# Performance work log

Hardware: AMD Instinct MI355X
Metric: run time of the kernel (lower is better)

Reference implementation:

```python
import jax, jax.numpy as jnp
import numpy as np

B, N, C = 2, 32768, 512
L, H = 64, 8
DH = C // H
NB = N // L
EG_HID = 16


def setup_inputs() -> dict:
    key = jax.random.key(0)
    ks = jax.random.split(key, 12)
    x = jax.random.normal(ks[0], (B, N, C), dtype=jnp.float32)
    attn_mask = jax.random.randint(ks[1], (NB, L, L), 0, 2, dtype=jnp.int32)
    edge_feats = jax.random.normal(ks[2], (NB, L, L, 4), dtype=jnp.float32)
    s = 1.0 / np.sqrt(C)
    w_qkv = jax.random.normal(ks[3], (C, 3 * C), dtype=jnp.float32) * s
    b_qkv = jnp.zeros((3 * C,), dtype=jnp.float32)
    w_proj = jax.random.normal(ks[4], (C, C), dtype=jnp.float32) * s
    b_proj = jnp.zeros((C,), dtype=jnp.float32)
    w_eg1 = jax.random.normal(ks[5], (4, EG_HID), dtype=jnp.float32) * 0.01
    b_eg1 = jnp.zeros((EG_HID,), dtype=jnp.float32)
    w_eg2 = jax.random.normal(ks[6], (EG_HID, H), dtype=jnp.float32) * 0.01
    b_eg2 = jnp.zeros((H,), dtype=jnp.float32)
    w_blk = jax.random.normal(ks[7], (C, H), dtype=jnp.float32) * 0.01
    b_blk = jnp.zeros((H,), dtype=jnp.float32)
    return {"x": x, "attn_mask": attn_mask, "edge_feats": edge_feats,
            "w_qkv": w_qkv, "b_qkv": b_qkv, "w_proj": w_proj, "b_proj": b_proj,
            "w_eg1": w_eg1, "b_eg1": b_eg1, "w_eg2": w_eg2, "b_eg2": b_eg2,
            "w_blk": w_blk, "b_blk": b_blk}


def reference(x, attn_mask, edge_feats, w_qkv, b_qkv, w_proj, b_proj,
              w_eg1, b_eg1, w_eg2, b_eg2, w_blk, b_blk):
    scale = DH ** -0.5
    x_blk = x.reshape(B, NB, L, C)
    # bias_physics: (B, NB, L, L, 4), expanded across batch
    bias = jnp.broadcast_to(edge_feats[None], (B, NB, L, L, 4))
    idx = jnp.arange(L)
    # zero diagonal, set channel 3 of diagonal to 1
    bias = bias.at[:, :, idx, idx, :].set(0.0)
    bias = bias.at[:, :, idx, idx, 3].set(1.0)
    # mask: (B, NB, L, L); ensure each query row attends to at least itself
    mask = jnp.broadcast_to(attn_mask[None], (B, NB, L, L))
    need_diag = (mask.sum(axis=-1) < 1).astype(mask.dtype)  # (B, NB, L)
    diag = mask[:, :, idx, idx]
    mask = mask.at[:, :, idx, idx].set(jnp.maximum(diag, need_diag))
    # qkv
    qkv = x_blk @ w_qkv + b_qkv  # (B, NB, L, 3C)
    q = qkv[..., :C].reshape(B, NB, L, H, DH)
    k = qkv[..., C:2 * C].reshape(B, NB, L, H, DH)
    v = qkv[..., 2 * C:].reshape(B, NB, L, H, DH)
    scores = jnp.einsum('bnqhd,bnkhd->bnqkh', q, k) * scale
    scores = scores + bias[..., 3:4]
    mask_e = (mask[..., None] == 0)  # (B, NB, L, L, 1)
    scores = jnp.where(mask_e, -jnp.inf, scores)
    attn_probs = jax.nn.softmax(scores, axis=3)
    # edge-gate MLP: 4 -> 16 (exact GELU) -> H
    gate = jax.nn.gelu(bias @ w_eg1 + b_eg1, approximate=False) @ w_eg2 + b_eg2
    gate = jnp.where(mask_e, 0.0, gate)
    combined = attn_probs + gate
    x_mid = jnp.einsum('bnqkh,bnkhd->bnqhd', combined, v)  # (B, NB, L, H, DH)
    # block route token
    block_node = x_blk.mean(axis=2, keepdims=True)  # (B, NB, 1, C)
    v_block = (block_node @ w_qkv + b_qkv)[..., 2 * C:].reshape(B, NB, 1, H, DH)
    g_block = jax.nn.sigmoid(x_blk @ w_blk + b_blk)  # (B, NB, L, H)
    x_mid = x_mid + g_block[..., None] * v_block
    out = x_mid.reshape(B, NB, L, C) @ w_proj + b_proj
    return out.reshape(B, N, C)
```

## Files before the change

kernel.cpp:

```cpp
#include <hip/hip_runtime.h>

typedef unsigned short u16;
typedef __attribute__((ext_vector_type(8))) short bf16x8;
typedef __attribute__((ext_vector_type(4))) float f32x4;

#define NTOK 32768
#define CC 512
#define HH 8
#define LL 64
#define NBLK 512
#define MTOK 65536

__device__ __forceinline__ u16 f2bf(float f) {
    unsigned int u = __float_as_uint(f);
    unsigned int r = u + 0x7fffu + ((u >> 16) & 1u);
    return (u16)(r >> 16);
}
__device__ __forceinline__ float bf2f(u16 h) {
    return __uint_as_float(((unsigned int)h) << 16);
}
__device__ __forceinline__ bf16x8 bc8(uint4 v) {
    return __builtin_bit_cast(bf16x8, v);
}
__device__ __forceinline__ void dma16(const u16* g, u16* l) {
    __builtin_amdgcn_global_load_lds((const __attribute__((address_space(1))) void*)g,
                                     (__attribute__((address_space(3))) void*)l, 16, 0, 0);
}

__global__ __launch_bounds__(256) void convert_gblock_kernel(const float* __restrict__ x,
                                                             u16* __restrict__ xbf,
                                                             const float* __restrict__ w_blk,
                                                             const float* __restrict__ b_blk,
                                                             float* __restrict__ gbl) {
    __shared__ float wbs[4608];
    int tid = threadIdx.x;
    for (int i = tid; i < 4096; i += 256) wbs[i + (i >> 6)] = w_blk[i];
    size_t tok = (size_t)blockIdx.x * 4 + (tid >> 6);
    int lane = tid & 63;
    int c0 = lane * 8;
    const float4* p = (const float4*)(x + tok * CC + c0);
    float4 a = p[0], b = p[1];
    uint4 o;
    o.x = (unsigned)f2bf(a.x) | ((unsigned)f2bf(a.y) << 16);
    o.y = (unsigned)f2bf(a.z) | ((unsigned)f2bf(a.w) << 16);
    o.z = (unsigned)f2bf(b.x) | ((unsigned)f2bf(b.y) << 16);
    o.w = (unsigned)f2bf(b.z) | ((unsigned)f2bf(b.w) << 16);
    *(uint4*)(xbf + tok * CC + c0) = o;
    float xv[8] = {a.x, a.y, a.z, a.w, b.x, b.y, b.z, b.w};
    __syncthreads();
    float acc[8];
#pragma unroll
    for (int h = 0; h < 8; ++h) acc[h] = 0.f;
#pragma unroll
    for (int j = 0; j < 8; ++j) {
        const float* wr = &wbs[(c0 + j) * 8 + lane];
#pragma unroll
        for (int h = 0; h < 8; ++h) acc[h] += xv[j] * wr[h];
    }
#pragma unroll
    for (int h = 0; h < 8; ++h) {
#pragma unroll
        for (int off = 1; off < 64; off <<= 1) acc[h] += __shfl_xor(acc[h], off);
    }
    float v = acc[0];
#pragma unroll
    for (int h = 1; h < 8; ++h) v = (lane == h) ? acc[h] : v;
    if (lane < 8) gbl[tok * 8 + lane] = 1.f / (1.f + __expf(-(v + b_blk[lane])));
}

__global__ __launch_bounds__(256) void transpose_bf16_kernel(const float* __restrict__ in,
                                                             u16* __restrict__ out,
                                                             int K, int Nn) {
    __shared__ float tile[32][33];
    int n0 = blockIdx.x * 32, k0 = blockIdx.y * 32;
    int tx = threadIdx.x & 31, ty = threadIdx.x >> 5;
#pragma unroll
    for (int i = 0; i < 4; ++i)
        tile[ty + i * 8][tx] = in[(size_t)(k0 + ty + i * 8) * Nn + n0 + tx];
    __syncthreads();
#pragma unroll
    for (int i = 0; i < 4; ++i)
        out[(size_t)(n0 + ty + i * 8) * K + k0 + tx] = f2bf(tile[tx][ty + i * 8]);
}

__global__ __launch_bounds__(256) void gate_sbias_kernel(const int* __restrict__ mask,
                                                         const float* __restrict__ edge,
                                                         const float* __restrict__ w1,
                                                         const float* __restrict__ b1,
                                                         const float* __restrict__ w2,
                                                         const float* __restrict__ b2,
                                                         u16* __restrict__ gate2,
                                                         u16* __restrict__ sbias2) {
    __shared__ float w1s[64], b1s[16], w2s[128], b2s[8];
    __shared__ int nds[16];
    int t = threadIdx.x;
    int nb = blockIdx.x >> 2;
    int qt = blockIdx.x & 3;
    if (t < 64) w1s[t] = w1[t];
    if (t < 16) b1s[t] = b1[t];
    if (t < 128) w2s[t] = w2[t];
    if (t < 8) b2s[t] = b2[t];
    if (t >= 128 && t < 144) {
        int q = qt * 16 + (t - 128);
        int s = 0;
        const int* mr = mask + (size_t)(nb * 64 + q) * 64;
#pragma unroll 8
        for (int k = 0; k < 64; ++k) s += mr[k];
        nds[t - 128] = (s < 1) ? 1 : 0;
    }
    __syncthreads();
#pragma unroll 1
    for (int it = 0; it < 4; ++it) {
        int p = it * 256 + t;
        int ql = p >> 6, k = p & 63;
        int q = qt * 16 + ql;
        int pk = (k & 15) * 4 + (k >> 4);
        int mv = mask[(size_t)(nb * 64 + q) * 64 + k];
        float e0, e1, e2, e3;
        if (q == k) {
            mv = max(mv, nds[ql]);
            e0 = e1 = e2 = 0.f;
            e3 = 1.f;
        } else {
            const float* ep = edge + ((size_t)(nb * 64 + q) * 64 + k) * 4;
            e0 = ep[0]; e1 = ep[1]; e2 = ep[2]; e3 = ep[3];
        }
        sbias2[(size_t)(nb * 64 + q) * 64 + pk] = f2bf(mv ? e3 : -1e30f);
        float g[8];
#pragma unroll
        for (int hh = 0; hh < 8; ++hh) g[hh] = b2s[hh];
#pragma unroll
        for (int j = 0; j < 16; ++j) {
            float hpre = e0 * w1s[j] + e1 * w1s[16 + j] + e2 * w1s[32 + j] + e3 * w1s[48 + j] + b1s[j];
            float hg = 0.5f * hpre * (1.f + erff(hpre * 0.70710678f));
#pragma unroll
            for (int hh = 0; hh < 8; ++hh) g[hh] += hg * w2s[j * 8 + hh];
        }
#pragma unroll
        for (int hh = 0; hh < 8; ++hh)
            gate2[(((size_t)nb * 8 + hh) * 64 + q) * 64 + pk] = f2bf(mv ? g[hh] : 0.f);
    }
}

__global__ __launch_bounds__(512, 4) void fused_qkv_attn_kernel(const u16* __restrict__ xbf,
                                                                const u16* __restrict__ wqkvT,
                                                                const float* __restrict__ b_qkv,
                                                                const u16* __restrict__ sbias2,
                                                                const u16* __restrict__ gate2,
                                                                const float* __restrict__ gbl,
                                                                u16* __restrict__ xmid) {
    __shared__ __align__(16) u16 Xs[2][64 * 64];
    __shared__ __align__(16) u16 QPs[2][64 * 72];
    __shared__ __align__(16) u16 Ks[2][64 * 72];
    __shared__ __align__(16) u16 VTs[2][64 * 72];
    __shared__ float gl[2][64], vbl[2][64];

    int tid = threadIdx.x;
    int bidf = blockIdx.x;
    int logical = (bidf & 7) * 512 + (bidf >> 3);
    int hp = logical & 3, nb = (logical >> 2) & 511, b = logical >> 11;
    int wave = tid >> 6, lane = tid & 63, l15 = lane & 15, quad = lane >> 4;
    int hloc = wave >> 2;
    int h = hp * 2 + hloc;
    int nt = wave & 3;
    int m0 = nt * 16;
    size_t blockrow = (size_t)(b * NTOK + nb * 64);

    int srow = tid >> 3;
    int jch = tid & 7;
    int js = jch ^ (srow & 7);
    const u16* gA = xbf + (blockrow + srow) * CC + js * 8;
    int sw = l15 & 7;

    const u16* gB0 = wqkvT + (size_t)(0 * 512 + h * 64 + nt * 16 + l15) * CC;
    const u16* gB1 = wqkvT + (size_t)(1 * 512 + h * 64 + nt * 16 + l15) * CC;
    const u16* gB2 = wqkvT + (size_t)(2 * 512 + h * 64 + nt * 16 + l15) * CC;
    float bq0 = b_qkv[0 * 512 + h * 64 + nt * 16 + l15];
    float bq1 = b_qkv[1 * 512 + h * 64 + nt * 16 + l15];
    float bq2 = b_qkv[2 * 512 + h * 64 + nt * 16 + l15];

    f32x4 accQ[4], accK[4], accV[4];
#pragma unroll
    for (int i = 0; i < 4; ++i) {
        accQ[i] = (f32x4){0.f, 0.f, 0.f, 0.f};
        accK[i] = (f32x4){0.f, 0.f, 0.f, 0.f};
        accV[i] = (f32x4){0.f, 0.f, 0.f, 0.f};
    }

    dma16(gA, &Xs[0][wave * 512]);
    __syncthreads();
    for (int kt = 0; kt < 8; ++kt) {
        int buf = kt & 1;
        if (kt < 7) dma16(gA + (kt + 1) * 64, &Xs[buf ^ 1][wave * 512]);
#pragma unroll
        for (int kk = 0; kk < 2; ++kk) {
            int ch = ((kk * 4 + quad) ^ sw) * 8;
            bf16x8 a[4];
#pragma unroll
            for (int i = 0; i < 4; ++i) a[i] = *(const bf16x8*)&Xs[buf][(i * 16 + l15) * 64 + ch];
            int ko = kt * 64 + kk * 32 + quad * 8;
            bf16x8 b0 = bc8(*(const uint4*)(gB0 + ko));
            bf16x8 b1 = bc8(*(const uint4*)(gB1 + ko));
            bf16x8 b2 = bc8(*(const uint4*)(gB2 + ko));
#pragma unroll
            for (int i = 0; i < 4; ++i) {
                accQ[i] = __builtin_amdgcn_mfma_f32_16x16x32_bf16(a[i], b0, accQ[i], 0, 0, 0);
                accK[i] = __builtin_amdgcn_mfma_f32_16x16x32_bf16(a[i], b1, accK[i], 0, 0, 0);
                accV[i] = __builtin_amdgcn_mfma_f32_16x16x32_bf16(a[i], b2, accV[i], 0, 0, 0);
            }
        }
        __syncthreads();
    }

    {
        int dloc = nt * 16 + l15;
#pragma unroll
        for (int i = 0; i < 4; ++i) {
#pragma unroll
            for (int r = 0; r < 4; ++r) {
                int tok = i * 16 + quad * 4 + r;
                QPs[hloc][tok * 72 + dloc] = f2bf(accQ[i][r] + bq0);
                Ks[hloc][tok * 72 + dloc] = f2bf(accK[i][r] + bq1);
                VTs[hloc][dloc * 72 + tok] = f2bf(accV[i][r] + bq2);
            }
        }
    }
    if (tid < 128) {
        int hl = tid >> 6, tok = tid & 63;
        gl[hl][tok] = gbl[(blockrow + tok) * 8 + hp * 2 + hl];
    }
    __syncthreads();

    if (tid < 128) {
        int hl = tid >> 6, d = tid & 63;
        float s = 0.f;
#pragma unroll 8
        for (int k = 0; k < 64; ++k) s += bf2f(VTs[hl][d * 72 + k]);
        vbl[hl][d] = s * 0.015625f;
    }

    f32x4 sc[4];
#pragma unroll
    for (int t = 0; t < 4; ++t) sc[t] = (f32x4){0.f, 0.f, 0.f, 0.f};
#pragma unroll
    for (int kk = 0; kk < 2; ++kk) {
        bf16x8 a = *(const bf16x8*)&QPs[hloc][(m0 + l15) * 72 + kk * 32 + quad * 8];
#pragma unroll
        for (int t = 0; t < 4; ++t) {
            bf16x8 bb = *(const bf16x8*)&Ks[hloc][(t * 16 + l15) * 72 + kk * 32 + quad * 8];
            sc[t] = __builtin_amdgcn_mfma_f32_16x16x32_bf16(a, bb, sc[t], 0, 0, 0);
        }
    }
    {
        const u16* sb2 = sbias2 + (size_t)nb * 4096;
        const u16* gp2 = gate2 + ((size_t)nb * 8 + h) * 4096;
#pragma unroll
        for (int r = 0; r < 4; ++r) {
            int q = m0 + quad * 4 + r;
            ushort4 sv = *(const ushort4*)(sb2 + (q * 16 + l15) * 4);
            float bias_t[4] = {bf2f(sv.x), bf2f(sv.y), bf2f(sv.z), bf2f(sv.w)};
            float mx = -3e38f;
#pragma unroll
            for (int t = 0; t < 4; ++t) {
                float v = sc[t][r] * 0.125f + bias_t[t];
                sc[t][r] = v;
                mx = fmaxf(mx, v);
            }
            mx = fmaxf(mx, __shfl_xor(mx, 1));
            mx = fmaxf(mx, __shfl_xor(mx, 2));
            mx = fmaxf(mx, __shfl_xor(mx, 4));
            mx = fmaxf(mx, __shfl_xor(mx, 8));
            float sum = 0.f;
#pragma unroll
            for (int t = 0; t < 4; ++t) {
                float p = __expf(sc[t][r] - mx);
                sc[t][r] = p;
                sum += p;
            }
            sum += __shfl_xor(sum, 1);
            sum += __shfl_xor(sum, 2);
            sum += __shfl_xor(sum, 4);
            sum += __shfl_xor(sum, 8);
            float inv = 1.f / sum;
            ushort4 gv = *(const ushort4*)(gp2 + (q * 16 + l15) * 4);
            float gate_t[4] = {bf2f(gv.x), bf2f(gv.y), bf2f(gv.z), bf2f(gv.w)};
#pragma unroll
            for (int t = 0; t < 4; ++t) {
                float comb = sc[t][r] * inv + gate_t[t];
                QPs[hloc][q * 72 + t * 16 + l15] = f2bf(comb);
            }
        }
    }
    __syncthreads();

    f32x4 o[4];
#pragma unroll
    for (int t = 0; t < 4; ++t) o[t] = (f32x4){0.f, 0.f, 0.f, 0.f};
#pragma unroll
    for (int kk = 0; kk < 2; ++kk) {
        bf16x8 a = *(const bf16x8*)&QPs[hloc][(m0 + l15) * 72 + kk * 32 + quad * 8];
#pragma unroll
        for (int t = 0; t < 4; ++t) {
            bf16x8 bb = *(const bf16x8*)&VTs[hloc][(t * 16 + l15) * 72 + kk * 32 + quad * 8];
            o[t] = __builtin_amdgcn_mfma_f32_16x16x32_bf16(a, bb, o[t], 0, 0, 0);
        }
    }
#pragma unroll
    for (int t = 0; t < 4; ++t) {
#pragma unroll
        for (int r = 0; r < 4; ++r) {
            int q = m0 + quad * 4 + r, d = t * 16 + l15;
            float v = o[t][r] + gl[hloc][q] * vbl[hloc][d];
            xmid[(blockrow + q) * CC + h * 64 + d] = f2bf(v);
        }
    }
}

__global__ __launch_bounds__(256) void outproj_kernel(const u16* __restrict__ xmid,
                                                      const u16* __restrict__ wprojT,
                                                      const float* __restrict__ b_proj,
                                                      float* __restrict__ out) {
    __shared__ __align__(16) u16 As[128 * 64], Bs[128 * 64];
    int tid = threadIdx.x;
    int flat = blockIdx.x;
    int logical = (flat & 7) * 256 + (flat >> 3);
    int n0 = (logical & 3) * 128;
    int m0 = (logical >> 2) * 128;
    int lane = tid & 63, l15 = lane & 15, quad = lane >> 4, wave = tid >> 6;
    int r8 = lane >> 3, jch = lane & 7;
    int js = jch ^ r8;
    int mwl = (wave >> 1) * 64, nwl = (wave & 1) * 64;
    int sw = l15 & 7;

    f32x4 acc[4][4];
#pragma unroll
    for (int i = 0; i < 4; ++i)
#pragma unroll
        for (int j = 0; j < 4; ++j) acc[i][j] = (f32x4){0.f, 0.f, 0.f, 0.f};

    int arow[4], brow[4];
#pragma unroll
    for (int i = 0; i < 4; ++i) arow[i] = (mwl + i * 16 + l15) * 64;
#pragma unroll
    for (int j = 0; j < 4; ++j) brow[j] = (nwl + j * 16 + l15) * 64;

    const u16* gA = xmid + (size_t)(m0 + wave * 32 + r8) * CC + js * 8;
    const u16* gB = wprojT + (size_t)(n0 + wave * 32 + r8) * CC + js * 8;
    u16* lA = As + wave * 32 * 64;
    u16* lB = Bs + wave * 32 * 64;

    for (int kt = 0; kt < 8; ++kt) {
        int k0 = kt * 64;
#pragma unroll
        for (int t = 0; t < 4; ++t) {
            dma16(gA + (size_t)t * 8 * CC + k0, lA + t * 8 * 64);
            dma16(gB + (size_t)t * 8 * CC + k0, lB + t * 8 * 64);
        }
        __syncthreads();
#pragma unroll
        for (int kk = 0; kk < 2; ++kk) {
            int ch = ((kk * 4 + quad) ^ sw) * 8;
            bf16x8 a[4], bb[4];
#pragma unroll
            for (int i = 0; i < 4; ++i) a[i] = *(const bf16x8*)&As[arow[i] + ch];
#pragma unroll
            for (int j = 0; j < 4; ++j) bb[j] = *(const bf16x8*)&Bs[brow[j] + ch];
#pragma unroll
            for (int i = 0; i < 4; ++i)
#pragma unroll
                for (int j = 0; j < 4; ++j)
                    acc[i][j] = __builtin_amdgcn_mfma_f32_16x16x32_bf16(a[i], bb[j], acc[i][j], 0, 0, 0);
        }
        __syncthreads();
    }
#pragma unroll
    for (int i = 0; i < 4; ++i)
#pragma unroll
        for (int j = 0; j < 4; ++j) {
            int col = n0 + nwl + j * 16 + l15;
            float bp = b_proj[col];
#pragma unroll
            for (int r = 0; r < 4; ++r) {
                int row = m0 + mwl + i * 16 + quad * 4 + r;
                out[(size_t)row * CC + col] = acc[i][j][r] + bp;
            }
        }
}

extern "C" void kernel_launch(void* const* d_in, const int* in_sizes, int n_in,
                              void* d_out, int out_size, void* d_ws, size_t ws_size,
                              hipStream_t stream) {
    const float* x = (const float*)d_in[0];
    const int* attn_mask = (const int*)d_in[1];
    const float* edge = (const float*)d_in[2];
    const float* w_qkv = (const float*)d_in[3];
    const float* b_qkv = (const float*)d_in[4];
    const float* w_proj = (const float*)d_in[5];
    const float* b_proj = (const float*)d_in[6];
    const float* w_eg1 = (const float*)d_in[7];
    const float* b_eg1 = (const float*)d_in[8];
    const float* w_eg2 = (const float*)d_in[9];
    const float* b_eg2 = (const float*)d_in[10];
    const float* w_blk = (const float*)d_in[11];
    const float* b_blk = (const float*)d_in[12];
    float* out = (float*)d_out;

    char* ws = (char*)d_ws;
    u16* xbf = (u16*)ws;
    u16* xmid = (u16*)(ws + 67108864);
    u16* gate2 = (u16*)(ws + 268435456);
    u16* sbias2 = (u16*)(ws + 301989888);
    u16* wqkvT = (u16*)(ws + 306184192);
    u16* wprojT = (u16*)(ws + 307757056);
    float* gbl = (float*)(ws + 308281344);

    convert_gblock_kernel<<<16384, 256, 0, stream>>>(x, xbf, w_blk, b_blk, gbl);
    transpose_bf16_kernel<<<dim3(48, 16), 256, 0, stream>>>(w_qkv, wqkvT, 512, 1536);
    transpose_bf16_kernel<<<dim3(16, 16), 256, 0, stream>>>(w_proj, wprojT, 512, 512);
    gate_sbias_kernel<<<2048, 256, 0, stream>>>(attn_mask, edge, w_eg1, b_eg1, w_eg2, b_eg2,
                                                gate2, sbias2);
    fused_qkv_attn_kernel<<<4096, 512, 0, stream>>>(xbf, wqkvT, b_qkv, sbias2, gate2, gbl, xmid);
    outproj_kernel<<<2048, 256, 0, stream>>>(xmid, wprojT, b_proj, out);
}
```

Measured before the change: 628.7 us.

## Software-pipeline QKV GEMM weight loads and prefetch bias/gate before softmax

Restructures the fused QKV projection main loop so the global weight fragments for the next k-step are loaded one step ahead into registers. The loop is fully unrolled and __syncthreads is replaced with explicit s_waitcnt vmcnt(3) plus s_barrier, so outstanding weight loads need not drain before the LDS double-buffer barrier. The score-bias and gate loads are also hoisted ahead of the score computation to hide their latency. The cost is higher register pressure, and correctness depends on the hand-counted vmcnt matching the number of in-flight loads.

New measurement: 642.2 us. 1.02x slower.

```diff
diff --git a/kernel.cpp b/kernel.cpp
--- a/kernel.cpp
+++ b/kernel.cpp
@@ -187,29 +187,106 @@
         accV[i] = (f32x4){0.f, 0.f, 0.f, 0.f};
     }
 
+    int koq = quad * 8;
     dma16(gA, &Xs[0][wave * 512]);
-    __syncthreads();
+    asm volatile("" ::: "memory");
+    bf16x8 c0 = bc8(*(const uint4*)(gB0 + koq));
+    bf16x8 c1 = bc8(*(const uint4*)(gB1 + koq));
+    bf16x8 c2 = bc8(*(const uint4*)(gB2 + koq));
+    asm volatile("s_waitcnt vmcnt(3)" ::: "memory");
+    __builtin_amdgcn_s_barrier();
+
+#pragma unroll
     for (int kt = 0; kt < 8; ++kt) {
         int buf = kt & 1;
-        if (kt < 7) dma16(gA + (kt + 1) * 64, &Xs[buf ^ 1][wave * 512]);
-#pragma unroll
-        for (int kk = 0; kk < 2; ++kk) {
-            int ch = ((kk * 4 + quad) ^ sw) * 8;
-            bf16x8 a[4];
-#pragma unroll
-            for (int i = 0; i < 4; ++i) a[i] = *(const bf16x8*)&Xs[buf][(i * 16 + l15) * 64 + ch];
-            int ko = kt * 64 + kk * 32 + quad * 8;
-            bf16x8 b0 = bc8(*(const uint4*)(gB0 + ko));
-            bf16x8 b1 = bc8(*(const uint4*)(gB1 + ko));
-            bf16x8 b2 = bc8(*(const uint4*)(gB2 + ko));
-#pragma unroll
-            for (int i = 0; i < 4; ++i) {
-                accQ[i] = __builtin_amdgcn_mfma_f32_16x16x32_bf16(a[i], b0, accQ[i], 0, 0, 0);
-                accK[i] = __builtin_amdgcn_mfma_f32_16x16x32_bf16(a[i], b1, accK[i], 0, 0, 0);
-                accV[i] = __builtin_amdgcn_mfma_f32_16x16x32_bf16(a[i], b2, accV[i], 0, 0, 0);
-            }
-        }
-        __syncthreads();
+        if (kt < 7) {
+            dma16(gA + (kt + 1) * 64, &Xs[buf ^ 1][wave * 512]);
+            asm volatile("" ::: "memory");
+        }
+        {
+            int ko1 = kt * 64 + 32 + koq;
+            bf16x8 n0 = bc8(*(const uint4*)(gB0 + ko1));
+            bf16x8 n1 = bc8(*(const uint4*)(gB1 + ko1));
+            bf16x8 n2 = bc8(*(const uint4*)(gB2 + ko1));
+            {
+                int ch = (quad ^ sw) * 8;
+                bf16x8 a0 = *(const bf16x8*)&Xs[buf][(0 * 16 + l15) * 64 + ch];
+                bf16x8 a1 = *(const bf16x8*)&Xs[buf][(1 * 16 + l15) * 64 + ch];
+                bf16x8 a2 = *(const bf16x8*)&Xs[buf][(2 * 16 + l15) * 64 + ch];
+                bf16x8 a3 = *(const bf16x8*)&Xs[buf][(3 * 16 + l15) * 64 + ch];
+                accQ[0] = __builtin_amdgcn_mfma_f32_16x16x32_bf16(a0, c0, accQ[0], 0, 0, 0);
+                accK[0] = __builtin_amdgcn_mfma_f32_16x16x32_bf16(a0, c1, accK[0], 0, 0, 0);
+                accV[0] = __builtin_amdgcn_mfma_f32_16x16x32_bf16(a0, c2, accV[0], 0, 0, 0);
+                accQ[1] = __builtin_amdgcn_mfma_f32_16x16x32_bf16(a1, c0, accQ[1], 0, 0, 0);
+                accK[1] = __builtin_amdgcn_mfma_f32_16x16x32_bf16(a1, c1, accK[1], 0, 0, 0);
+                accV[1] = __builtin_amdgcn_mfma_f32_16x16x32_bf16(a1, c2, accV[1], 0, 0, 0);
+                accQ[2] = __builtin_amdgcn_mfma_f32_16x16x32_bf16(a2, c0, accQ[2], 0, 0, 0);
+                accK[2] = __builtin_amdgcn_mfma_f32_16x16x32_bf16(a2, c1, accK[2], 0, 0, 0);
+                accV[2] = __builtin_amdgcn_mfma_f32_16x16x32_bf16(a2, c2, accV[2], 0, 0, 0);
+                accQ[3] = __builtin_amdgcn_mfma_f32_16x16x32_bf16(a3, c0, accQ[3], 0, 0, 0);
+                accK[3] = __builtin_amdgcn_mfma_f32_16x16x32_bf16(a3, c1, accK[3], 0, 0, 0);
+                accV[3] = __builtin_amdgcn_mfma_f32_16x16x32_bf16(a3, c2, accV[3], 0, 0, 0);
+            }
+            c0 = n0; c1 = n1; c2 = n2;
+        }
+        if (kt < 7) {
+            int ko2 = (kt + 1) * 64 + koq;
+            bf16x8 n0 = bc8(*(const uint4*)(gB0 + ko2));
+            bf16x8 n1 = bc8(*(const uint4*)(gB1 + ko2));
+            bf16x8 n2 = bc8(*(const uint4*)(gB2 + ko2));
+            {
+                int ch = ((4 + quad) ^ sw) * 8;
+                bf16x8 a0 = *(const bf16x8*)&Xs[buf][(0 * 16 + l15) * 64 + ch];
+                bf16x8 a1 = *(const bf16x8*)&Xs[buf][(1 * 16 + l15) * 64 + ch];
+                bf16x8 a2 = *(const bf16x8*)&Xs[buf][(2 * 16 + l15) * 64 + ch];
+                bf16x8 a3 = *(const bf16x8*)&Xs[buf][(3 * 16 + l15) * 64 + ch];
+                accQ[0] = __builtin_amdgcn_mfma_f32_16x16x32_bf16(a0, c0, accQ[0], 0, 0, 0);
+                accK[0] = __builtin_amdgcn_mfma_f32_16x16x32_bf16(a0, c1, accK[0], 0, 0, 0);
+                accV[0] = __builtin_amdgcn_mfma_f32_16x16x32_bf16(a0, c2, accV[0], 0, 0, 0);
+                accQ[1] = __builtin_amdgcn_mfma_f32_16x16x32_bf16(a1, c0, accQ[1], 0, 0, 0);
+                accK[1] = __builtin_amdgcn_mfma_f32_16x16x32_bf16(a1, c1, accK[1], 0, 0, 0);
+                accV[1] = __builtin_amdgcn_mfma_f32_16x16x32_bf16(a1, c2, accV[1], 0, 0, 0);
+                accQ[2] = __builtin_amdgcn_mfma_f32_16x16x32_bf16(a2, c0, accQ[2], 0, 0, 0);
+                accK[2] = __builtin_amdgcn_mfma_f32_16x16x32_bf16(a2, c1, accK[2], 0, 0, 0);
+                accV[2] = __builtin_amdgcn_mfma_f32_16x16x32_bf16(a2, c2, accV[2], 0, 0, 0);
+                accQ[3] = __builtin_amdgcn_mfma_f32_16x16x32_bf16(a3, c0, accQ[3], 0, 0, 0);
+                accK[3] = __builtin_amdgcn_mfma_f32_16x16x32_bf16(a3, c1, accK[3], 0, 0, 0);
+                accV[3] = __builtin_amdgcn_mfma_f32_16x16x32_bf16(a3, c2, accV[3], 0, 0, 0);
+            }
+            c0 = n0; c1 = n1; c2 = n2;
+            asm volatile("s_waitcnt vmcnt(3)" ::: "memory");
+            __builtin_amdgcn_s_barrier();
+        } else {
+            int ch = ((4 + quad) ^ sw) * 8;
+            bf16x8 a0 = *(const bf16x8*)&Xs[buf][(0 * 16 + l15) * 64 + ch];
+            bf16x8 a1 = *(const bf16x8*)&Xs[buf][(1 * 16 + l15) * 64 + ch];
+            bf16x8 a2 = *(const bf16x8*)&Xs[buf][(2 * 16 + l15) * 64 + ch];
+            bf16x8 a3 = *(const bf16x8*)&Xs[buf][(3 * 16 + l15) * 64 + ch];
+            accQ[0] = __builtin_amdgcn_mfma_f32_16x16x32_bf16(a0, c0, accQ[0], 0, 0, 0);
+            accK[0] = __builtin_amdgcn_mfma_f32_16x16x32_bf16(a0, c1, accK[0], 0, 0, 0);
+            accV[0] = __builtin_amdgcn_mfma_f32_16x16x32_bf16(a0, c2, accV[0], 0, 0, 0);
+            accQ[1] = __builtin_amdgcn_mfma_f32_16x16x32_bf16(a1, c0, accQ[1], 0, 0, 0);
+            accK[1] = __builtin_amdgcn_mfma_f32_16x16x32_bf16(a1, c1, accK[1], 0, 0, 0);
+            accV[1] = __builtin_amdgcn_mfma_f32_16x16x32_bf16(a1, c2, accV[1], 0, 0, 0);
+            accQ[2] = __builtin_amdgcn_mfma_f32_16x16x32_bf16(a2, c0, accQ[2], 0, 0, 0);
+            accK[2] = __builtin_amdgcn_mfma_f32_16x16x32_bf16(a2, c1, accK[2], 0, 0, 0);
+            accV[2] = __builtin_amdgcn_mfma_f32_16x16x32_bf16(a2, c2, accV[2], 0, 0, 0);
+            accQ[3] = __builtin_amdgcn_mfma_f32_16x16x32_bf16(a3, c0, accQ[3], 0, 0, 0);
+            accK[3] = __builtin_amdgcn_mfma_f32_16x16x32_bf16(a3, c1, accK[3], 0, 0, 0);
+            accV[3] = __builtin_amdgcn_mfma_f32_16x16x32_bf16(a3, c2, accV[3], 0, 0, 0);
+        }
+    }
+
+    ushort4 svp[4], gvp[4];
+    {
+        const u16* sb2 = sbias2 + (size_t)nb * 4096;
+        const u16* gp2 = gate2 + ((size_t)nb * 8 + h) * 4096;
+#pragma unroll
+        for (int r = 0; r < 4; ++r) {
+            int q = m0 + quad * 4 + r;
+            svp[r] = *(const ushort4*)(sb2 + (q * 16 + l15) * 4);
+            gvp[r] = *(const ushort4*)(gp2 + (q * 16 + l15) * 4);
+        }
     }
 
     {
@@ -252,12 +329,10 @@
         }
     }
     {
-        const u16* sb2 = sbias2 + (size_t)nb * 4096;
-        const u16* gp2 = gate2 + ((size_t)nb * 8 + h) * 4096;
 #pragma unroll
         for (int r = 0; r < 4; ++r) {
             int q = m0 + quad * 4 + r;
-            ushort4 sv = *(const ushort4*)(sb2 + (q * 16 + l15) * 4);
+            ushort4 sv = svp[r];
             float bias_t[4] = {bf2f(sv.x), bf2f(sv.y), bf2f(sv.z), bf2f(sv.w)};
             float mx = -3e38f;
 #pragma unroll
@@ -282,7 +357,7 @@
             sum += __shfl_xor(sum, 4);
             sum += __shfl_xor(sum, 8);
             float inv = 1.f / sum;
-            ushort4 gv = *(const ushort4*)(gp2 + (q * 16 + l15) * 4);
+            ushort4 gv = gvp[r];
             float gate_t[4] = {bf2f(gv.x), bf2f(gv.y), bf2f(gv.z), bf2f(gv.w)};
 #pragma unroll
             for (int t = 0; t < 4; ++t) {
```

## Split fused attention to one head per block and load X directly from global

Applied to the files above, without the earlier changes.

The fused QKV+attention kernel now handles one head per 256-thread block instead of two heads per 512-thread block, doubling the grid. The double-buffered LDS staging of the X tile and its per-iteration barriers are removed; each wave reads its A fragments straight from global memory. Sbias and gate loads are hoisted so they are issued before the softmax. In exchange, the X tile is re-read once per head, which raises global and L2 traffic, and the global loads are no longer explicitly overlapped with compute.

Measured after the change: 828.6 us. 31.8% more time.

```diff
diff --git a/kernel.cpp b/kernel.cpp
--- a/kernel.cpp
+++ b/kernel.cpp
@@ -142,39 +142,34 @@
     }
 }
 
-__global__ __launch_bounds__(512, 4) void fused_qkv_attn_kernel(const u16* __restrict__ xbf,
+__global__ __launch_bounds__(256, 5) void fused_qkv_attn_kernel(const u16* __restrict__ xbf,
                                                                 const u16* __restrict__ wqkvT,
                                                                 const float* __restrict__ b_qkv,
                                                                 const u16* __restrict__ sbias2,
                                                                 const u16* __restrict__ gate2,
                                                                 const float* __restrict__ gbl,
                                                                 u16* __restrict__ xmid) {
-    __shared__ __align__(16) u16 Xs[2][64 * 64];
-    __shared__ __align__(16) u16 QPs[2][64 * 72];
-    __shared__ __align__(16) u16 Ks[2][64 * 72];
-    __shared__ __align__(16) u16 VTs[2][64 * 72];
-    __shared__ float gl[2][64], vbl[2][64];
+    __shared__ __align__(16) u16 QPs[64 * 72];
+    __shared__ __align__(16) u16 Ks[64 * 72];
+    __shared__ __align__(16) u16 VTs[64 * 72];
+    __shared__ float gl[64], vbl[64];
 
     int tid = threadIdx.x;
     int bidf = blockIdx.x;
-    int logical = (bidf & 7) * 512 + (bidf >> 3);
-    int hp = logical & 3, nb = (logical >> 2) & 511, b = logical >> 11;
+    int logical = (bidf & 7) * 1024 + (bidf >> 3);
+    int h = logical & 7, nb = (logical >> 3) & 511, b = logical >> 12;
     int wave = tid >> 6, lane = tid & 63, l15 = lane & 15, quad = lane >> 4;
-    int hloc = wave >> 2;
-    int h = hp * 2 + hloc;
-    int nt = wave & 3;
+    int nt = wave;
     int m0 = nt * 16;
     size_t blockrow = (size_t)(b * NTOK + nb * 64);
 
-    int srow = tid >> 3;
-    int jch = tid & 7;
-    int js = jch ^ (srow & 7);
-    const u16* gA = xbf + (blockrow + srow) * CC + js * 8;
-    int sw = l15 & 7;
-
-    const u16* gB0 = wqkvT + (size_t)(0 * 512 + h * 64 + nt * 16 + l15) * CC;
-    const u16* gB1 = wqkvT + (size_t)(1 * 512 + h * 64 + nt * 16 + l15) * CC;
-    const u16* gB2 = wqkvT + (size_t)(2 * 512 + h * 64 + nt * 16 + l15) * CC;
+    const u16* gA0 = xbf + (blockrow + 0 * 16 + l15) * CC + quad * 8;
+    const u16* gA1 = xbf + (blockrow + 1 * 16 + l15) * CC + quad * 8;
+    const u16* gA2 = xbf + (blockrow + 2 * 16 + l15) * CC + quad * 8;
+    const u16* gA3 = xbf + (blockrow + 3 * 16 + l15) * CC + quad * 8;
+    const u16* gB0 = wqkvT + (size_t)(0 * 512 + h * 64 + nt * 16 + l15) * CC + quad * 8;
+    const u16* gB1 = wqkvT + (size_t)(1 * 512 + h * 64 + nt * 16 + l15) * CC + quad * 8;
+    const u16* gB2 = wqkvT + (size_t)(2 * 512 + h * 64 + nt * 16 + l15) * CC + quad * 8;
     float bq0 = b_qkv[0 * 512 + h * 64 + nt * 16 + l15];
     float bq1 = b_qkv[1 * 512 + h * 64 + nt * 16 + l15];
     float bq2 = b_qkv[2 * 512 + h * 64 + nt * 16 + l15];
@@ -187,77 +182,88 @@
         accV[i] = (f32x4){0.f, 0.f, 0.f, 0.f};
     }
 
-    dma16(gA, &Xs[0][wave * 512]);
-    __syncthreads();
+#pragma unroll 2
     for (int kt = 0; kt < 8; ++kt) {
-        int buf = kt & 1;
-        if (kt < 7) dma16(gA + (kt + 1) * 64, &Xs[buf ^ 1][wave * 512]);
 #pragma unroll
         for (int kk = 0; kk < 2; ++kk) {
-            int ch = ((kk * 4 + quad) ^ sw) * 8;
-            bf16x8 a[4];
-#pragma unroll
-            for (int i = 0; i < 4; ++i) a[i] = *(const bf16x8*)&Xs[buf][(i * 16 + l15) * 64 + ch];
-            int ko = kt * 64 + kk * 32 + quad * 8;
+            int ko = kt * 64 + kk * 32;
+            bf16x8 a0 = bc8(*(const uint4*)(gA0 + ko));
+            bf16x8 a1 = bc8(*(const uint4*)(gA1 + ko));
+            bf16x8 a2 = bc8(*(const uint4*)(gA2 + ko));
+            bf16x8 a3 = bc8(*(const uint4*)(gA3 + ko));
             bf16x8 b0 = bc8(*(const uint4*)(gB0 + ko));
             bf16x8 b1 = bc8(*(const uint4*)(gB1 + ko));
             bf16x8 b2 = bc8(*(const uint4*)(gB2 + ko));
-#pragma unroll
-            for (int i = 0; i < 4; ++i) {
-                accQ[i] = __builtin_amdgcn_mfma_f32_16x16x32_bf16(a[i], b0, accQ[i], 0, 0, 0);
-                accK[i] = __builtin_amdgcn_mfma_f32_16x16x32_bf16(a[i], b1, accK[i], 0, 0, 0);
-                accV[i] = __builtin_amdgcn_mfma_f32_16x16x32_bf16(a[i], b2, accV[i], 0, 0, 0);
-            }
-        }
-        __syncthreads();
-    }
-
-    {
-        int dloc = nt * 16 + l15;
-#pragma unroll
-        for (int i = 0; i < 4; ++i) {
-#pragma unroll
-            for (int r = 0; r < 4; ++r) {
-                int tok = i * 16 + quad * 4 + r;
-                QPs[hloc][tok * 72 + dloc] = f2bf(accQ[i][r] + bq0);
-                Ks[hloc][tok * 72 + dloc] = f2bf(accK[i][r] + bq1);
-                VTs[hloc][dloc * 72 + tok] = f2bf(accV[i][r] + bq2);
-            }
-        }
-    }
-    if (tid < 128) {
-        int hl = tid >> 6, tok = tid & 63;
-        gl[hl][tok] = gbl[(blockrow + tok) * 8 + hp * 2 + hl];
-    }
-    __syncthreads();
-
-    if (tid < 128) {
-        int hl = tid >> 6, d = tid & 63;
-        float s = 0.f;
-#pragma unroll 8
-        for (int k = 0; k < 64; ++k) s += bf2f(VTs[hl][d * 72 + k]);
-        vbl[hl][d] = s * 0.015625f;
-    }
-
-    f32x4 sc[4];
-#pragma unroll
-    for (int t = 0; t < 4; ++t) sc[t] = (f32x4){0.f, 0.f, 0.f, 0.f};
-#pragma unroll
-    for (int kk = 0; kk < 2; ++kk) {
-        bf16x8 a = *(const bf16x8*)&QPs[hloc][(m0 + l15) * 72 + kk * 32 + quad * 8];
-#pragma unroll
-        for (int t = 0; t < 4; ++t) {
-            bf16x8 bb = *(const bf16x8*)&Ks[hloc][(t * 16 + l15) * 72 + kk * 32 + quad * 8];
-            sc[t] = __builtin_amdgcn_mfma_f32_16x16x32_bf16(a, bb, sc[t], 0, 0, 0);
-        }
-    }
+            accQ[0] = __builtin_amdgcn_mfma_f32_16x16x32_bf16(a0, b0, accQ[0], 0, 0, 0);
+            accK[0] = __builtin_amdgcn_mfma_f32_16x16x32_bf16(a0, b1, accK[0], 0, 0, 0);
+            accV[0] = __builtin_amdgcn_mfma_f32_16x16x32_bf16(a0, b2, accV[0], 0, 0, 0);
+            accQ[1] = __builtin_amdgcn_mfma_f32_16x16x32_bf16(a1, b0, accQ[1], 0, 0, 0);
+            accK[1] = __builtin_amdgcn_mfma_f32_16x16x32_bf16(a1, b1, accK[1], 0, 0, 0);
+            accV[1] = __builtin_amdgcn_mfma_f32_16x16x32_bf16(a1, b2, accV[1], 0, 0, 0);
+            accQ[2] = __builtin_amdgcn_mfma_f32_16x16x32_bf16(a2, b0, accQ[2], 0, 0, 0);
+            accK[2] = __builtin_amdgcn_mfma_f32_16x16x32_bf16(a2, b1, accK[2], 0, 0, 0);
+            accV[2] = __builtin_amdgcn_mfma_f32_16x16x32_bf16(a2, b2, accV[2], 0, 0, 0);
+            accQ[3] = __builtin_amdgcn_mfma_f32_16x16x32_bf16(a3, b0, accQ[3], 0, 0, 0);
+            accK[3] = __builtin_amdgcn_mfma_f32_16x16x32_bf16(a3, b1, accK[3], 0, 0, 0);
+            accV[3] = __builtin_amdgcn_mfma_f32_16x16x32_bf16(a3, b2, accV[3], 0, 0, 0);
+        }
+    }
+
+    ushort4 svp[4], gvp[4];
     {
         const u16* sb2 = sbias2 + (size_t)nb * 4096;
         const u16* gp2 = gate2 + ((size_t)nb * 8 + h) * 4096;
 #pragma unroll
         for (int r = 0; r < 4; ++r) {
             int q = m0 + quad * 4 + r;
-            ushort4 sv = *(const ushort4*)(sb2 + (q * 16 + l15) * 4);
+            svp[r] = *(const ushort4*)(sb2 + (q * 16 + l15) * 4);
+            gvp[r] = *(const ushort4*)(gp2 + (q * 16 + l15) * 4);
+        }
+    }
+
+    {
+        int dloc = nt * 16 + l15;
+#pragma unroll
+        for (int i = 0; i < 4; ++i) {
+#pragma unroll
+            for (int r = 0; r < 4; ++r) {
+                int tok = i * 16 + quad * 4 + r;
+                QPs[tok * 72 + dloc] = f2bf(accQ[i][r] + bq0);
+                Ks[tok * 72 + dloc] = f2bf(accK[i][r] + bq1);
+                VTs[dloc * 72 + tok] = f2bf(accV[i][r] + bq2);
+            }
+        }
+    }
+    if (tid >= 64 && tid < 128) {
+        int tok = tid & 63;
+        gl[tok] = gbl[(blockrow + tok) * 8 + h];
+    }
+    __syncthreads();
+
+    if (tid < 64) {
+        float s = 0.f;
+#pragma unroll 8
+        for (int k = 0; k < 64; ++k) s += bf2f(VTs[tid * 72 + k]);
+        vbl[tid] = s * 0.015625f;
+    }
+
+    f32x4 sc[4];
+#pragma unroll
+    for (int t = 0; t < 4; ++t) sc[t] = (f32x4){0.f, 0.f, 0.f, 0.f};
+#pragma unroll
+    for (int kk = 0; kk < 2; ++kk) {
+        bf16x8 a = *(const bf16x8*)&QPs[(m0 + l15) * 72 + kk * 32 + quad * 8];
+#pragma unroll
+        for (int t = 0; t < 4; ++t) {
+            bf16x8 bb = *(const bf16x8*)&Ks[(t * 16 + l15) * 72 + kk * 32 + quad * 8];
+            sc[t] = __builtin_amdgcn_mfma_f32_16x16x32_bf16(a, bb, sc[t], 0, 0, 0);
+        }
+    }
+    {
+#pragma unroll
+        for (int r = 0; r < 4; ++r) {
+            int q = m0 + quad * 4 + r;
+            ushort4 sv = svp[r];
             float bias_t[4] = {bf2f(sv.x), bf2f(sv.y), bf2f(sv.z), bf2f(sv.w)};
             float mx = -3e38f;
 #pragma unroll
@@ -282,12 +288,12 @@
             sum += __shfl_xor(sum, 4);
             sum += __shfl_xor(sum, 8);
             float inv = 1.f / sum;
-            ushort4 gv = *(const ushort4*)(gp2 + (q * 16 + l15) * 4);
+            ushort4 gv = gvp[r];
             float gate_t[4] = {bf2f(gv.x), bf2f(gv.y), bf2f(gv.z), bf2f(gv.w)};
 #pragma unroll
             for (int t = 0; t < 4; ++t) {
                 float comb = sc[t][r] * inv + gate_t[t];
-                QPs[hloc][q * 72 + t * 16 + l15] = f2bf(comb);
+                QPs[q * 72 + t * 16 + l15] = f2bf(comb);
             }
         }
     }
@@ -298,10 +304,10 @@
     for (int t = 0; t < 4; ++t) o[t] = (f32x4){0.f, 0.f, 0.f, 0.f};
 #pragma unroll
     for (int kk = 0; kk < 2; ++kk) {
-        bf16x8 a = *(const bf16x8*)&QPs[hloc][(m0 + l15) * 72 + kk * 32 + quad * 8];
+        bf16x8 a = *(const bf16x8*)&QPs[(m0 + l15) * 72 + kk * 32 + quad * 8];
 #pragma unroll
         for (int t = 0; t < 4; ++t) {
-            bf16x8 bb = *(const bf16x8*)&VTs[hloc][(t * 16 + l15) * 72 + kk * 32 + quad * 8];
+            bf16x8 bb = *(const bf16x8*)&VTs[(t * 16 + l15) * 72 + kk * 32 + quad * 8];
             o[t] = __builtin_amdgcn_mfma_f32_16x16x32_bf16(a, bb, o[t], 0, 0, 0);
         }
     }
@@ -310,7 +316,7 @@
 #pragma unroll
         for (int r = 0; r < 4; ++r) {
             int q = m0 + quad * 4 + r, d = t * 16 + l15;
-            float v = o[t][r] + gl[hloc][q] * vbl[hloc][d];
+            float v = o[t][r] + gl[q] * vbl[d];
             xmid[(blockrow + q) * CC + h * 64 + d] = f2bf(v);
         }
     }
@@ -419,6 +425,6 @@
     transpose_bf16_kernel<<<dim3(16, 16), 256, 0, stream>>>(w_proj, wprojT, 512, 512);
     gate_sbias_kernel<<<2048, 256, 0, stream>>>(attn_mask, edge, w_eg1, b_eg1, w_eg2, b_eg2,
                                                 gate2, sbias2);
-    fused_qkv_attn_kernel<<<4096, 512, 0, stream>>>(xbf, wqkvT, b_qkv, sbias2, gate2, gbl, xmid);
+    fused_qkv_attn_kernel<<<8192, 256, 0, stream>>>(xbf, wqkvT, b_qkv, sbias2, gate2, gbl, xmid);
     outproj_kernel<<<2048, 256, 0, stream>>>(xmid, wprojT, b_proj, out);
 }
```
